# Kernel optimization log

Hardware: AMD Instinct MI355X
Metric: run time of the kernel (lower is better)

## Reference

```python
import jax, jax.numpy as jnp
import numpy as np

C = 256
CQK = C // 8  # 32

def setup_inputs() -> dict:
    key = jax.random.key(0)
    ks = jax.random.split(key, 9)
    B, H, W = 4, 64, 64
    shp = (B, C, H, W)
    v = jax.random.normal(ks[0], shp, dtype=jnp.float32)
    k = jax.random.normal(ks[1], shp, dtype=jnp.float32)
    q = jax.random.normal(ks[2], shp, dtype=jnp.float32)
    s = 1.0 / np.sqrt(C)
    Wq = jax.random.normal(ks[3], (CQK, C), dtype=jnp.float32) * s
    bq = jnp.zeros((CQK,), dtype=jnp.float32)
    Wk = jax.random.normal(ks[4], (CQK, C), dtype=jnp.float32) * s
    bk = jnp.zeros((CQK,), dtype=jnp.float32)
    Wv = jax.random.normal(ks[5], (C, C), dtype=jnp.float32) * s
    bv = jnp.zeros((C,), dtype=jnp.float32)
    # torch inits gamma=0 (out == v); use small nonzero so attention path is exercised
    gamma = jnp.full((1,), 0.5, dtype=jnp.float32)
    return {"v": v, "k": k, "q": q, "Wq": Wq, "bq": bq, "Wk": Wk, "bk": bk,
            "Wv": Wv, "bv": bv, "gamma": gamma}

def reference(v, k, q, Wq, bq, Wk, bk, Wv, bv, gamma):
    B, Cc, Hh, Ww = v.shape
    N = Hh * Ww
    # 1x1 convs == per-pixel channel matmuls
    pq = jnp.einsum('oc,bchw->bohw', Wq, q) + bq[None, :, None, None]  # B,CQK,H,W
    pk = jnp.einsum('oc,bchw->bohw', Wk, k) + bk[None, :, None, None]
    pv = jnp.einsum('oc,bchw->bohw', Wv, v) + bv[None, :, None, None]  # B,C,H,W
    pq = pq.reshape(B, -1, N)  # B,d,N
    pk = pk.reshape(B, -1, N)
    pv = pv.reshape(B, Cc, N)
    # energy[b,n,m] = <q_n, k_m>; softmax over m (keys)
    energy = jnp.einsum('bdn,bdm->bnm', pq, pk)
    attn = jax.nn.softmax(energy, axis=-1)
    # out[b,c,n] = sum_m v[b,c,m] * attn[b,n,m]
    out = jnp.einsum('bcm,bnm->bcn', pv, attn).reshape(B, Cc, Hh, Ww)
    return gamma * out + v
```

## Files before the change

kernel.cpp:

```cpp
#include <hip/hip_runtime.h>
#include <hip/hip_bf16.h>

typedef __attribute__((ext_vector_type(8))) short short8_t;
typedef __attribute__((ext_vector_type(4))) short short4_t;
typedef __attribute__((ext_vector_type(4))) float float4_t;

#define B_   4
#define C_   256
#define N_   4096
#define DQK  32
#define LOG2E 1.4426950408889634f

#define VMCNT4   asm volatile("s_waitcnt vmcnt(4)" ::: "memory")
#define VMCNT0   asm volatile("s_waitcnt vmcnt(0)" ::: "memory")
#define LGKM0    asm volatile("s_waitcnt lgkmcnt(0)" ::: "memory")
#define SBAR     __builtin_amdgcn_s_barrier()
#define SCHEDB   __builtin_amdgcn_sched_barrier(0)

__device__ __forceinline__ unsigned short f2bf(float x) {
    union { float f; unsigned int u; } v; v.f = x;
    unsigned int r = v.u + 0x7FFFu + ((v.u >> 16) & 1u);
    return (unsigned short)(r >> 16);
}
__device__ __forceinline__ unsigned short f2bf_hw(float x) {
    return __bfloat16_as_ushort(__float2bfloat16(x));
}

__global__ __launch_bounds__(256) void cast_w_k(
        const float* __restrict__ Wq, const float* __restrict__ Wk,
        const float* __restrict__ Wv,
        unsigned short* __restrict__ Wqb, unsigned short* __restrict__ Wkb,
        unsigned short* __restrict__ Wvb) {
    int i = blockIdx.x * 256 + threadIdx.x;
    if (i < 8192)            Wqb[i] = f2bf(Wq[i]);
    else if (i < 16384)      Wkb[i - 8192] = f2bf(Wk[i - 8192]);
    else                     Wvb[i - 16384] = f2bf(Wv[i - 16384]);
}

__global__ __launch_bounds__(256) void proj_qk_k(
        const float* __restrict__ q_in, const float* __restrict__ k_in,
        const unsigned short* __restrict__ Wqb, const unsigned short* __restrict__ Wkb,
        const float* __restrict__ bq, const float* __restrict__ bk,
        unsigned short* __restrict__ pqT, unsigned short* __restrict__ pkT) {
    int b = blockIdx.y, z = blockIdx.z;
    const float* X = z ? k_in : q_in;
    const unsigned short* W = z ? Wkb : Wqb;
    const float* bias = z ? bk : bq;
    unsigned short* P = z ? pkT : pqT;
    float scl = z ? 1.0f : LOG2E;
    int tid = threadIdx.x, wave = tid >> 6, lane = tid & 63, l15 = lane & 15, g = lane >> 4;
    int nb = blockIdx.x * 64 + wave * 16;
    float4_t acc0 = {0.f, 0.f, 0.f, 0.f}, acc1 = {0.f, 0.f, 0.f, 0.f};
    const float* Xcol = X + (size_t)b * C_ * N_ + nb + l15;
#pragma unroll
    for (int kk = 0; kk < 8; ++kk) {
        short8_t a;
#pragma unroll
        for (int j = 0; j < 8; ++j)
            a[j] = (short)f2bf(Xcol[(size_t)(kk * 32 + 8 * g + j) * N_]);
        short8_t b0 = *(const short8_t*)(W + (size_t)l15 * C_ + kk * 32 + 8 * g);
        short8_t b1 = *(const short8_t*)(W + (size_t)(16 + l15) * C_ + kk * 32 + 8 * g);
        acc0 = __builtin_amdgcn_mfma_f32_16x16x32_bf16(a, b0, acc0, 0, 0, 0);
        acc1 = __builtin_amdgcn_mfma_f32_16x16x32_bf16(a, b1, acc1, 0, 0, 0);
    }
#pragma unroll
    for (int r = 0; r < 4; ++r) {
        int n = nb + 4 * g + r;
        P[((size_t)b * N_ + n) * DQK + l15]      = f2bf((acc0[r] + bias[l15]) * scl);
        P[((size_t)b * N_ + n) * DQK + 16 + l15] = f2bf((acc1[r] + bias[16 + l15]) * scl);
    }
}

__global__ __launch_bounds__(256) void proj_v_k(
        const float* __restrict__ v_in, const unsigned short* __restrict__ Wvb,
        const float* __restrict__ bv, unsigned short* __restrict__ pv) {
    int b = blockIdx.y;
    int tid = threadIdx.x, wave = tid >> 6, lane = tid & 63, l15 = lane & 15, g = lane >> 4;
    int mb = blockIdx.x * 16;
    int m = mb + l15;
    int k32 = m & 31;
    int pcol = (k32 < 16) ? ((k32 >> 2) * 8 + (k32 & 3))
                          : (((k32 - 16) >> 2) * 8 + 4 + (k32 & 3));
    int mcol = (m & ~31) + pcol;
    float4_t acc[4];
#pragma unroll
    for (int i = 0; i < 4; ++i) acc[i] = (float4_t){0.f, 0.f, 0.f, 0.f};
    const float* Vcol = v_in + (size_t)b * C_ * N_ + mb + l15;
#pragma unroll
    for (int kk = 0; kk < 8; ++kk) {
        short8_t bf;
#pragma unroll
        for (int j = 0; j < 8; ++j)
            bf[j] = (short)f2bf(Vcol[(size_t)(kk * 32 + 8 * g + j) * N_]);
#pragma unroll
        for (int ct = 0; ct < 4; ++ct) {
            short8_t af = *(const short8_t*)(Wvb + (size_t)(wave * 64 + ct * 16 + l15) * C_ + kk * 32 + 8 * g);
            acc[ct] = __builtin_amdgcn_mfma_f32_16x16x32_bf16(af, bf, acc[ct], 0, 0, 0);
        }
    }
#pragma unroll
    for (int ct = 0; ct < 4; ++ct)
#pragma unroll
        for (int r = 0; r < 4; ++r) {
            int c = wave * 64 + ct * 16 + 4 * g + r;
            pv[((size_t)b * C_ + c) * N_ + mcol] = f2bf(acc[ct][r] + bv[c]);
        }
}

__global__ __launch_bounds__(256, 2) void attn_split_k(
        const unsigned short* __restrict__ pqT, const unsigned short* __restrict__ pkT,
        const unsigned short* __restrict__ pv,
        float* __restrict__ accP, float* __restrict__ lP, int KS) {
    __shared__ __align__(16) unsigned short VT[2][256][64];
    int nqb = gridDim.x;
    int lin = blockIdx.x + nqb * (blockIdx.y + KS * blockIdx.z);
    int cpx = (nqb * KS * 4) >> 3;
    int sl  = (lin & 7) * cpx + (lin >> 3);
    int qbi = sl % nqb;
    int s   = (sl / nqb) % KS;
    int b   = sl / (nqb * KS);

    int kps = N_ / KS, ks0 = s * kps, nt = kps >> 6;
    int tid = threadIdx.x, wave = tid >> 6, lane = tid & 63, l15 = lane & 15, g = lane >> 4;
    int qb = qbi * 64;
    int sw = (l15 & 7) << 4;
    int rl = lane >> 3, cl = (lane & 7) ^ rl;

    short8_t qf = *(const short8_t*)(pqT + ((size_t)b * N_ + qb + wave * 16 + l15) * DQK + 8 * g);
    float4_t acc[16];
#pragma unroll
    for (int i = 0; i < 16; ++i) acc[i] = (float4_t){0.f, 0.f, 0.f, 0.f};
    float4_t accl = {0.f, 0.f, 0.f, 0.f};
    short8_t onef;
#pragma unroll
    for (int j = 0; j < 8; ++j) onef[j] = (short)0x3F80;
    const float4_t zero4 = {0.f, 0.f, 0.f, 0.f};
    const unsigned short* pvb = pv + (size_t)b * C_ * N_;
    const char* pkTb = (const char*)pkT + (size_t)b * N_ * DQK * 2;

    unsigned soff[8];
#pragma unroll
    for (int i = 0; i < 8; ++i)
        soff[i] = (unsigned)(((wave * 64 + i * 8 + rl) * N_ + ks0 + 8 * cl) * 2);
    unsigned koff = (unsigned)(((ks0 + l15) * DQK + 8 * g) * 2);
    int off1 = (16 * g) ^ sw, off2 = (64 + 16 * g) ^ sw;
    const char* vbA = (const char*)&VT[0][0][0] + l15 * 128 + off1;
    const char* vbB = (const char*)&VT[0][0][0] + l15 * 128 + off2;

#define STAGE(RBUF)                                                           \
    _Pragma("unroll")                                                         \
    for (int i_ = 0; i_ < 8; ++i_) {                                          \
        __builtin_amdgcn_global_load_lds(                                     \
            (const __attribute__((address_space(1))) unsigned int*)(const void*)((const char*)pvb + soff[i_]), \
            (__attribute__((address_space(3))) unsigned int*)(void*)&VT[RBUF][wave * 64 + i_ * 8][0], 16, 0, 0); \
    }                                                                          \
    _Pragma("unroll")                                                         \
    for (int i_ = 0; i_ < 8; ++i_) soff[i_] += 128;

#define KFLOAD(DST)                                                           \
    _Pragma("unroll")                                                         \
    for (int it_ = 0; it_ < 4; ++it_)                                         \
        DST[it_] = *(const short8_t*)(pkTb + koff + it_ * 1024);              \
    koff += 4096;

#define QKEXP(KF, PN0, PN1)                                                   \
    {                                                                          \
        float4_t sv_[4];                                                       \
        _Pragma("unroll")                                                      \
        for (int it_ = 0; it_ < 4; ++it_)                                      \
            sv_[it_] = __builtin_amdgcn_mfma_f32_16x16x32_bf16(KF[it_], qf, zero4, 0, 0, 0); \
        float p_[16];                                                          \
        _Pragma("unroll")                                                      \
        for (int it_ = 0; it_ < 4; ++it_)                                      \
            _Pragma("unroll")                                                  \
            for (int r_ = 0; r_ < 4; ++r_)                                     \
                p_[it_ * 4 + r_] = exp2f(sv_[it_][r_]);                        \
        _Pragma("unroll")                                                      \
        for (int j_ = 0; j_ < 4; ++j_) {                                       \
            PN0[j_]     = (short)f2bf_hw(p_[j_]);                              \
            PN0[4 + j_] = (short)f2bf_hw(p_[4 + j_]);                          \
            PN1[j_]     = (short)f2bf_hw(p_[8 + j_]);                          \
            PN1[4 + j_] = (short)f2bf_hw(p_[12 + j_]);                         \
        }                                                                      \
    }

#define PVPH(RB, PC0, PC1)                                                    \
    __builtin_amdgcn_s_setprio(1);                                            \
    _Pragma("unroll")                                                         \
    for (int ct_ = 0; ct_ < 16; ++ct_) {                                      \
        short8_t va0_ = *(const short8_t*)(vbA + (RB) * 32768 + ct_ * 2048);  \
        short8_t va1_ = *(const short8_t*)(vbB + (RB) * 32768 + ct_ * 2048);  \
        acc[ct_] = __builtin_amdgcn_mfma_f32_16x16x32_bf16(va0_, PC0, acc[ct_], 0, 0, 0); \
        acc[ct_] = __builtin_amdgcn_mfma_f32_16x16x32_bf16(va1_, PC1, acc[ct_], 0, 0, 0); \
    }                                                                          \
    accl = __builtin_amdgcn_mfma_f32_16x16x32_bf16(onef, PC0, accl, 0, 0, 0); \
    accl = __builtin_amdgcn_mfma_f32_16x16x32_bf16(onef, PC1, accl, 0, 0, 0); \
    __builtin_amdgcn_s_setprio(0);

#define BODY(RB, KFC, KFN, PC0, PC1, PN0, PN1, TT)                            \
    if ((TT) + 1 < nt) { STAGE(RB ^ 1) }                                      \
    SCHEDB;                                                                   \
    KFLOAD(KFN)                                                               \
    QKEXP(KFC, PN0, PN1)                                                      \
    PVPH(RB, PC0, PC1)                                                        \
    LGKM0; SCHEDB;                                                            \
    SBAR;                                                                     \
    VMCNT4; SCHEDB;                                                           \
    SBAR;

    short8_t kfA[4], kfB[4];
    short8_t pbA0, pbA1, pbB0, pbB1;
    STAGE(0)
    SCHEDB;
    KFLOAD(kfB)
    KFLOAD(kfA)
    VMCNT0; SCHEDB;
    QKEXP(kfB, pbB0, pbB1)
    SBAR;

    for (int t = 0; t < nt; t += 2) {
        BODY(0, kfA, kfB, pbB0, pbB1, pbA0, pbA1, t)
        BODY(1, kfB, kfA, pbA0, pbA1, pbB0, pbB1, t + 1)
    }

    if (g == 0)
        lP[(size_t)(b * KS + s) * N_ + qb + wave * 16 + l15] = accl[0];
    float* accOut = accP + ((size_t)(b * KS + s) * C_) * N_;
#pragma unroll
    for (int ct = 0; ct < 16; ++ct)
#pragma unroll
        for (int r = 0; r < 4; ++r) {
            int c = ct * 16 + 4 * g + r;
            accOut[(size_t)c * N_ + qb + wave * 16 + l15] = acc[ct][r];
        }
#undef STAGE
#undef KFLOAD
#undef QKEXP
#undef PVPH
#undef BODY
}

__global__ __launch_bounds__(256) void combine_k(
        const float* __restrict__ accP, const float* __restrict__ lP,
        const float* __restrict__ v_in, const float* __restrict__ gamma,
        float* __restrict__ out, int KS) {
    int i = blockIdx.x * 256 + threadIdx.x;
    const int nq4 = N_ / 4;
    int q0 = (i % nq4) * 4;
    int c  = (i / nq4) % C_;
    int b  = i / (nq4 * C_);
    float4_t num = {0.f, 0.f, 0.f, 0.f}, den = {0.f, 0.f, 0.f, 0.f};
    for (int s = 0; s < KS; ++s) {
        float4_t l4 = *(const float4_t*)(lP + (size_t)(b * KS + s) * N_ + q0);
        float4_t a4 = *(const float4_t*)(accP + ((size_t)(b * KS + s) * C_ + c) * N_ + q0);
#pragma unroll
        for (int j = 0; j < 4; ++j) {
            den[j] += l4[j];
            num[j] += a4[j];
        }
    }
    float gm = gamma[0];
    size_t idx = ((size_t)(b * C_ + c)) * N_ + q0;
    float4_t vi = *(const float4_t*)(v_in + idx);
    float4_t o;
#pragma unroll
    for (int j = 0; j < 4; ++j) o[j] = gm * num[j] / den[j] + vi[j];
    *(float4_t*)(out + idx) = o;
}

extern "C" void kernel_launch(void* const* d_in, const int* in_sizes, int n_in,
                              void* d_out, int out_size, void* d_ws, size_t ws_size,
                              hipStream_t stream) {
    (void)in_sizes; (void)n_in; (void)out_size;
    const float* v_in  = (const float*)d_in[0];
    const float* k_in  = (const float*)d_in[1];
    const float* q_in  = (const float*)d_in[2];
    const float* Wq    = (const float*)d_in[3];
    const float* bq    = (const float*)d_in[4];
    const float* Wk    = (const float*)d_in[5];
    const float* bk    = (const float*)d_in[6];
    const float* Wv    = (const float*)d_in[7];
    const float* bv    = (const float*)d_in[8];
    const float* gamma = (const float*)d_in[9];
    float* out = (float*)d_out;

    char* ws = (char*)d_ws;
    unsigned short* pvb = (unsigned short*)(ws + 0);
    unsigned short* pqT = (unsigned short*)(ws + 8388608);
    unsigned short* pkT = (unsigned short*)(ws + 9437184);
    unsigned short* Wqb = (unsigned short*)(ws + 10502144);
    unsigned short* Wkb = (unsigned short*)(ws + 10518528);
    unsigned short* Wvb = (unsigned short*)(ws + 10534912);
    const size_t base2 = 10665984;

    int KS = 2;
    while (KS > 1) {
        size_t need = base2 + (size_t)KS * 16777216 + (size_t)KS * 262144;
        if (need <= ws_size) break;
        KS >>= 1;
    }
    float* accP = (float*)(ws + base2);
    float* lP   = (float*)(ws + base2 + (size_t)KS * 16777216);

    cast_w_k<<<320, 256, 0, stream>>>(Wq, Wk, Wv, Wqb, Wkb, Wvb);
    proj_qk_k<<<dim3(64, 4, 2), 256, 0, stream>>>(q_in, k_in, Wqb, Wkb, bq, bk, pqT, pkT);
    proj_v_k<<<dim3(256, 4), 256, 0, stream>>>(v_in, Wvb, bv, pvb);
    attn_split_k<<<dim3(64, KS, 4), 256, 0, stream>>>(pqT, pkT, pvb, accP, lP, KS);
    combine_k<<<4096, 256, 0, stream>>>(accP, lP, v_in, gamma, out, KS);
}
```

Before: 101.4 us.

## Swap attention work split: waves own channel slices, share P via LDS

The split-K attention kernel is restructured so each wave owns 64 output channels for all 64 queries, instead of 16 queries across all 256 channels. V tiles are loaded straight from global memory into registers, with no staging in LDS. The small bf16 probability tiles are written to a double-buffered LDS array and read back by every wave. This cuts LDS traffic, since P is far smaller than the V tile, and removes the vmcnt waits tied to the async global-to-LDS copies. In exchange, V arrives through plain global loads that must be hidden by register double-buffering, and every wave now re-reads P and must cross a barrier each step.

Result: slower. 130.1 us (+28.4%).

```diff
diff --git a/kernel.cpp b/kernel.cpp
--- a/kernel.cpp
+++ b/kernel.cpp
@@ -11,8 +11,6 @@
 #define DQK  32
 #define LOG2E 1.4426950408889634f
 
-#define VMCNT4   asm volatile("s_waitcnt vmcnt(4)" ::: "memory")
-#define VMCNT0   asm volatile("s_waitcnt vmcnt(0)" ::: "memory")
 #define LGKM0    asm volatile("s_waitcnt lgkmcnt(0)" ::: "memory")
 #define SBAR     __builtin_amdgcn_s_barrier()
 #define SCHEDB   __builtin_amdgcn_sched_barrier(0)
@@ -111,7 +109,7 @@
         const unsigned short* __restrict__ pqT, const unsigned short* __restrict__ pkT,
         const unsigned short* __restrict__ pv,
         float* __restrict__ accP, float* __restrict__ lP, int KS) {
-    __shared__ __align__(16) unsigned short VT[2][256][64];
+    __shared__ __align__(16) short8_t Pl[2][4][2][4][16];
     int nqb = gridDim.x;
     int lin = blockIdx.x + nqb * (blockIdx.y + KS * blockIdx.z);
     int cpx = (nqb * KS * 4) >> 3;
@@ -123,39 +121,37 @@
     int kps = N_ / KS, ks0 = s * kps, nt = kps >> 6;
     int tid = threadIdx.x, wave = tid >> 6, lane = tid & 63, l15 = lane & 15, g = lane >> 4;
     int qb = qbi * 64;
-    int sw = (l15 & 7) << 4;
-    int rl = lane >> 3, cl = (lane & 7) ^ rl;
 
     short8_t qf = *(const short8_t*)(pqT + ((size_t)b * N_ + qb + wave * 16 + l15) * DQK + 8 * g);
-    float4_t acc[16];
-#pragma unroll
-    for (int i = 0; i < 16; ++i) acc[i] = (float4_t){0.f, 0.f, 0.f, 0.f};
+    float4_t acc[4][4];
+#pragma unroll
+    for (int i = 0; i < 4; ++i)
+#pragma unroll
+        for (int j = 0; j < 4; ++j) acc[i][j] = (float4_t){0.f, 0.f, 0.f, 0.f};
     float4_t accl = {0.f, 0.f, 0.f, 0.f};
     short8_t onef;
 #pragma unroll
     for (int j = 0; j < 8; ++j) onef[j] = (short)0x3F80;
     const float4_t zero4 = {0.f, 0.f, 0.f, 0.f};
-    const unsigned short* pvb = pv + (size_t)b * C_ * N_;
+    const char* pvb8 = (const char*)(pv + (size_t)b * C_ * N_);
     const char* pkTb = (const char*)pkT + (size_t)b * N_ * DQK * 2;
 
-    unsigned soff[8];
-#pragma unroll
-    for (int i = 0; i < 8; ++i)
-        soff[i] = (unsigned)(((wave * 64 + i * 8 + rl) * N_ + ks0 + 8 * cl) * 2);
+    unsigned voff[4][2];
+#pragma unroll
+    for (int ct = 0; ct < 4; ++ct)
+#pragma unroll
+        for (int kh = 0; kh < 2; ++kh)
+            voff[ct][kh] = (unsigned)((((wave * 64 + ct * 16 + l15) * N_) + ks0 + kh * 32 + 8 * g) * 2);
     unsigned koff = (unsigned)(((ks0 + l15) * DQK + 8 * g) * 2);
-    int off1 = (16 * g) ^ sw, off2 = (64 + 16 * g) ^ sw;
-    const char* vbA = (const char*)&VT[0][0][0] + l15 * 128 + off1;
-    const char* vbB = (const char*)&VT[0][0][0] + l15 * 128 + off2;
-
-#define STAGE(RBUF)                                                           \
+
+#define VLOAD(DST)                                                            \
     _Pragma("unroll")                                                         \
-    for (int i_ = 0; i_ < 8; ++i_) {                                          \
-        __builtin_amdgcn_global_load_lds(                                     \
-            (const __attribute__((address_space(1))) unsigned int*)(const void*)((const char*)pvb + soff[i_]), \
-            (__attribute__((address_space(3))) unsigned int*)(void*)&VT[RBUF][wave * 64 + i_ * 8][0], 16, 0, 0); \
-    }                                                                          \
-    _Pragma("unroll")                                                         \
-    for (int i_ = 0; i_ < 8; ++i_) soff[i_] += 128;
+    for (int ct_ = 0; ct_ < 4; ++ct_)                                         \
+        _Pragma("unroll")                                                     \
+        for (int kh_ = 0; kh_ < 2; ++kh_) {                                   \
+            DST[ct_][kh_] = *(const short8_t*)(pvb8 + voff[ct_][kh_]);        \
+            voff[ct_][kh_] += 128;                                            \
+        }
 
 #define KFLOAD(DST)                                                           \
     _Pragma("unroll")                                                         \
@@ -163,7 +159,7 @@
         DST[it_] = *(const short8_t*)(pkTb + koff + it_ * 1024);              \
     koff += 4096;
 
-#define QKEXP(KF, PN0, PN1)                                                   \
+#define QKWR(KF, NB)                                                          \
     {                                                                          \
         float4_t sv_[4];                                                       \
         _Pragma("unroll")                                                      \
@@ -175,68 +171,84 @@
             _Pragma("unroll")                                                  \
             for (int r_ = 0; r_ < 4; ++r_)                                     \
                 p_[it_ * 4 + r_] = exp2f(sv_[it_][r_]);                        \
+        short8_t pbn0_, pbn1_;                                                 \
         _Pragma("unroll")                                                      \
         for (int j_ = 0; j_ < 4; ++j_) {                                       \
-            PN0[j_]     = (short)f2bf_hw(p_[j_]);                              \
-            PN0[4 + j_] = (short)f2bf_hw(p_[4 + j_]);                          \
-            PN1[j_]     = (short)f2bf_hw(p_[8 + j_]);                          \
-            PN1[4 + j_] = (short)f2bf_hw(p_[12 + j_]);                         \
+            pbn0_[j_]     = (short)f2bf_hw(p_[j_]);                            \
+            pbn0_[4 + j_] = (short)f2bf_hw(p_[4 + j_]);                        \
+            pbn1_[j_]     = (short)f2bf_hw(p_[8 + j_]);                        \
+            pbn1_[4 + j_] = (short)f2bf_hw(p_[12 + j_]);                       \
         }                                                                      \
-    }
-
-#define PVPH(RB, PC0, PC1)                                                    \
-    __builtin_amdgcn_s_setprio(1);                                            \
+        accl = __builtin_amdgcn_mfma_f32_16x16x32_bf16(onef, pbn0_, accl, 0, 0, 0); \
+        accl = __builtin_amdgcn_mfma_f32_16x16x32_bf16(onef, pbn1_, accl, 0, 0, 0); \
+        Pl[NB][wave][0][g][l15] = pbn0_;                                       \
+        Pl[NB][wave][1][g][l15] = pbn1_;                                       \
+    }
+
+#define PFREAD(DST, CB, QT0)                                                  \
     _Pragma("unroll")                                                         \
-    for (int ct_ = 0; ct_ < 16; ++ct_) {                                      \
-        short8_t va0_ = *(const short8_t*)(vbA + (RB) * 32768 + ct_ * 2048);  \
-        short8_t va1_ = *(const short8_t*)(vbB + (RB) * 32768 + ct_ * 2048);  \
-        acc[ct_] = __builtin_amdgcn_mfma_f32_16x16x32_bf16(va0_, PC0, acc[ct_], 0, 0, 0); \
-        acc[ct_] = __builtin_amdgcn_mfma_f32_16x16x32_bf16(va1_, PC1, acc[ct_], 0, 0, 0); \
-    }                                                                          \
-    accl = __builtin_amdgcn_mfma_f32_16x16x32_bf16(onef, PC0, accl, 0, 0, 0); \
-    accl = __builtin_amdgcn_mfma_f32_16x16x32_bf16(onef, PC1, accl, 0, 0, 0); \
-    __builtin_amdgcn_s_setprio(0);
-
-#define BODY(RB, KFC, KFN, PC0, PC1, PN0, PN1, TT)                            \
-    if ((TT) + 1 < nt) { STAGE(RB ^ 1) }                                      \
-    SCHEDB;                                                                   \
-    KFLOAD(KFN)                                                               \
-    QKEXP(KFC, PN0, PN1)                                                      \
-    PVPH(RB, PC0, PC1)                                                        \
-    LGKM0; SCHEDB;                                                            \
-    SBAR;                                                                     \
-    VMCNT4; SCHEDB;                                                           \
+    for (int q2_ = 0; q2_ < 2; ++q2_)                                         \
+        _Pragma("unroll")                                                     \
+        for (int kh_ = 0; kh_ < 2; ++kh_)                                     \
+            DST[q2_][kh_] = Pl[CB][(QT0) + q2_][kh_][g][l15];
+
+#define PVM(VS, PF, QT0)                                                      \
+    _Pragma("unroll")                                                         \
+    for (int ct_ = 0; ct_ < 4; ++ct_)                                         \
+        _Pragma("unroll")                                                     \
+        for (int q2_ = 0; q2_ < 2; ++q2_) {                                   \
+            acc[ct_][(QT0) + q2_] = __builtin_amdgcn_mfma_f32_16x16x32_bf16(VS[ct_][0], PF[q2_][0], acc[ct_][(QT0) + q2_], 0, 0, 0); \
+            acc[ct_][(QT0) + q2_] = __builtin_amdgcn_mfma_f32_16x16x32_bf16(VS[ct_][1], PF[q2_][1], acc[ct_][(QT0) + q2_], 0, 0, 0); \
+        }
+
+#define BODY(T, VS, KF, CB, NB)                                               \
+    {                                                                          \
+        short8_t pfA_[2][2], pfB_[2][2];                                       \
+        PFREAD(pfA_, CB, 0)                                                    \
+        if ((T) + 1 < nt) { QKWR(KF, NB) }                                     \
+        KFLOAD(KF)                                                             \
+        PFREAD(pfB_, CB, 2)                                                    \
+        __builtin_amdgcn_s_setprio(1);                                         \
+        PVM(VS, pfA_, 0)                                                       \
+        PVM(VS, pfB_, 2)                                                       \
+        __builtin_amdgcn_s_setprio(0);                                         \
+        VLOAD(VS)                                                              \
+        LGKM0; SCHEDB;                                                         \
+        SBAR;                                                                  \
+    }
+
+    short8_t vX[4][2], vY[4][2], kfA[4], kfB[4];
+    VLOAD(vX)
+    KFLOAD(kfA)
+    VLOAD(vY)
+    KFLOAD(kfB)
+    QKWR(kfA, 0)
+    KFLOAD(kfA)
+    LGKM0; SCHEDB;
     SBAR;
 
-    short8_t kfA[4], kfB[4];
-    short8_t pbA0, pbA1, pbB0, pbB1;
-    STAGE(0)
-    SCHEDB;
-    KFLOAD(kfB)
-    KFLOAD(kfA)
-    VMCNT0; SCHEDB;
-    QKEXP(kfB, pbB0, pbB1)
-    SBAR;
-
     for (int t = 0; t < nt; t += 2) {
-        BODY(0, kfA, kfB, pbB0, pbB1, pbA0, pbA1, t)
-        BODY(1, kfB, kfA, pbA0, pbA1, pbB0, pbB1, t + 1)
+        BODY(t,     vX, kfB, 0, 1)
+        BODY(t + 1, vY, kfA, 1, 0)
     }
 
     if (g == 0)
         lP[(size_t)(b * KS + s) * N_ + qb + wave * 16 + l15] = accl[0];
     float* accOut = accP + ((size_t)(b * KS + s) * C_) * N_;
 #pragma unroll
-    for (int ct = 0; ct < 16; ++ct)
-#pragma unroll
-        for (int r = 0; r < 4; ++r) {
-            int c = ct * 16 + 4 * g + r;
-            accOut[(size_t)c * N_ + qb + wave * 16 + l15] = acc[ct][r];
-        }
-#undef STAGE
+    for (int ct = 0; ct < 4; ++ct)
+#pragma unroll
+        for (int qt = 0; qt < 4; ++qt)
+#pragma unroll
+            for (int r = 0; r < 4; ++r) {
+                int c = wave * 64 + ct * 16 + 4 * g + r;
+                accOut[(size_t)c * N_ + qb + qt * 16 + l15] = acc[ct][qt][r];
+            }
+#undef VLOAD
 #undef KFLOAD
-#undef QKEXP
-#undef PVPH
+#undef QKWR
+#undef PFREAD
+#undef PVM
 #undef BODY
 }
 
```
